# Performance work log

Measured on AMD Instinct MI355X. Metric: run time of the kernel, lower is better.

## Reference

```python
import jax, jax.numpy as jnp
import numpy as np

L, CH, S = 4096, 512, 64
SAMPLE_RATE = 4096.0


def setup_inputs() -> dict:
    key = jax.random.key(0)
    kx, ka, kc = jax.random.split(key, 3)
    x = jax.random.normal(kx, (L, CH), dtype=jnp.float32)
    # original init: lognegA = log(arange(1..S)) broadcast over channels; any real values work
    lognegA = jnp.broadcast_to(jnp.log(jnp.arange(1, S + 1, dtype=jnp.float32)), (CH, S)) \
        + 0.0 * jax.random.normal(ka, (CH, S), dtype=jnp.float32)
    B = jnp.ones((CH, S), dtype=jnp.float32)
    C = 0.01 * jax.random.normal(kc, (CH, S), dtype=jnp.float32)  # nn.initializers.normal() stddev=0.01
    return {"x": x, "lognegA": lognegA, "B": B, "C": C}


def reference(x, lognegA, B, C):
    length = x.shape[0]
    dt = 1.0 / SAMPLE_RATE
    A = -jnp.exp(lognegA)                         # [C, S], strictly negative
    Bd = (jnp.exp(A * dt) - 1.0) * B / A          # discretized B, [C, S]
    # Vandermonde-style kernel: Ak[l, c, s] = exp(l * A[c, s] * dt)
    Ak = jnp.exp(jnp.einsum('l,cs->lcs', jnp.arange(length, dtype=x.dtype), A * dt))
    K = jnp.einsum('cs,lcs->lc', C * Bd, Ak)      # [L, C] per-channel kernel
    # per-channel full causal convolution, truncated to length
    y = jax.vmap(jnp.convolve, in_axes=1, out_axes=1)(x, K)[:length]
    return y
```

## Files before the change

kernel.cpp:

```cpp
#include <hip/hip_runtime.h>


namespace {

constexpr int L_ = 4096;
constexpr int CH_ = 512;
constexpr int S_ = 64;
constexpr float DT = 1.0f / 4096.0f;
constexpr int SC = S_ * CH_;

__global__ void k_params(const float* __restrict__ lognegA,
                         const float* __restrict__ B,
                         const float* __restrict__ C,
                         float* __restrict__ rt, float* __restrict__ wt) {
  const int tid = blockIdx.x * blockDim.x + threadIdx.x;
  const int s = tid >> 9;
  const int c = tid & (CH_ - 1);
  const int i = c * S_ + s;
  const float A = -expf(lognegA[i]);
  const float r = expf(A * DT);
  rt[tid] = r;
  wt[tid] = C[i] * ((r - 1.0f) * B[i] / A);
}

template <int T>
__global__ __launch_bounds__(64) void k_local(const float* __restrict__ x,
                                              const float* __restrict__ rt,
                                              float* __restrict__ carry) {
  const int c = blockIdx.x * 64 + threadIdx.x;
  const int k = blockIdx.y;

  float r[S_], h[S_];
#pragma unroll
  for (int s = 0; s < S_; ++s) {
    r[s] = rt[s * CH_ + c];
    h[s] = 0.0f;
  }

  const float* xp = x + (size_t)k * T * CH_ + c;
#pragma unroll 4
  for (int l = 0; l < T; ++l) {
    const float xv = xp[l * CH_];
#pragma unroll
    for (int s = 0; s < S_; ++s) h[s] = fmaf(r[s], h[s], xv);
  }

  float* cp = carry + (size_t)k * SC + c;
#pragma unroll
  for (int s = 0; s < S_; ++s) cp[s * CH_] = h[s];
}

template <int T, int NC>
__global__ void k_combine(const float* __restrict__ rt,
                          float* __restrict__ carry) {
  const int tid = blockIdx.x * blockDim.x + threadIdx.x;

  const float r = rt[tid];
  float rT = r;
#pragma unroll
  for (int t = 1; t < T; t <<= 1) rT *= rT;

  constexpr int BATCH = (NC < 32) ? NC : 32;
  float state = 0.0f;
  for (int kb = 0; kb < NC; kb += BATCH) {
    float v[BATCH];
#pragma unroll
    for (int j = 0; j < BATCH; ++j) v[j] = carry[(size_t)(kb + j) * SC + tid];
#pragma unroll
    for (int j = 0; j < BATCH; ++j) {
      const float le = v[j];
      v[j] = state;
      state = fmaf(rT, state, le);
    }
#pragma unroll
    for (int j = 0; j < BATCH; ++j) carry[(size_t)(kb + j) * SC + tid] = v[j];
  }
}

template <int T, bool USE_CARRY>
__global__ __launch_bounds__(64) void k_scan_out(const float* __restrict__ x,
                                                 const float* __restrict__ rt,
                                                 const float* __restrict__ wt,
                                                 const float* __restrict__ carry,
                                                 float* __restrict__ y) {
  const int c = blockIdx.x * 64 + threadIdx.x;
  const int k = blockIdx.y;

  float r[S_], w[S_], h[S_];
#pragma unroll
  for (int s = 0; s < S_; ++s) {
    r[s] = rt[s * CH_ + c];
    w[s] = wt[s * CH_ + c];
    h[s] = USE_CARRY ? carry[(size_t)k * SC + s * CH_ + c] : 0.0f;
  }

  const float* xp = x + (size_t)k * T * CH_ + c;
  float* yp = y + (size_t)k * T * CH_ + c;

#pragma unroll 4
  for (int l = 0; l < T; ++l) {
    const float xv = xp[l * CH_];
    float acc[8] = {0, 0, 0, 0, 0, 0, 0, 0};
#pragma unroll
    for (int s = 0; s < S_; ++s) {
      h[s] = fmaf(r[s], h[s], xv);
      acc[s & 7] = fmaf(w[s], h[s], acc[s & 7]);
    }
    yp[l * CH_] = ((acc[0] + acc[4]) + (acc[2] + acc[6])) +
                  ((acc[1] + acc[5]) + (acc[3] + acc[7]));
  }
}

template <int T>
void launch_all(const float* x, const float* la, const float* B, const float* C,
                float* ws, float* y, hipStream_t stream) {
  constexpr int NC = L_ / T;
  float* carry = ws;
  float* rt = ws + (size_t)NC * SC;
  float* wt = rt + SC;

  k_params<<<SC / 256, 256, 0, stream>>>(la, B, C, rt, wt);
  dim3 g(CH_ / 64, NC);
  if (NC > 1) {
    k_local<T><<<g, 64, 0, stream>>>(x, rt, carry);
    k_combine<T, NC><<<SC / 256, 256, 0, stream>>>(rt, carry);
    k_scan_out<T, true><<<g, 64, 0, stream>>>(x, rt, wt, carry, y);
  } else {
    k_scan_out<T, false><<<g, 64, 0, stream>>>(x, rt, wt, carry, y);
  }
}

}

extern "C" void kernel_launch(void* const* d_in, const int* in_sizes, int n_in,
                              void* d_out, int out_size, void* d_ws, size_t ws_size,
                              hipStream_t stream) {
  const float* x = (const float*)d_in[0];
  const float* la = (const float*)d_in[1];
  const float* B = (const float*)d_in[2];
  const float* C = (const float*)d_in[3];
  float* y = (float*)d_out;
  float* ws = (float*)d_ws;

  int NC = 128;
  while (NC > 1 &&
         ((size_t)NC * SC + 2 * SC) * sizeof(float) > ws_size) NC >>= 1;

  switch (L_ / NC) {
    case 32:   launch_all<32>(x, la, B, C, ws, y, stream); break;
    case 64:   launch_all<64>(x, la, B, C, ws, y, stream); break;
    case 128:  launch_all<128>(x, la, B, C, ws, y, stream); break;
    case 256:  launch_all<256>(x, la, B, C, ws, y, stream); break;
    case 512:  launch_all<512>(x, la, B, C, ws, y, stream); break;
    case 1024: launch_all<1024>(x, la, B, C, ws, y, stream); break;
    case 2048: launch_all<2048>(x, la, B, C, ws, y, stream); break;
    default:   launch_all<4096>(x, la, B, C, ws, y, stream); break;
  }
}
```

Before: 95.85 us.

## Split state dimension across four wavefronts and reduce outputs through LDS

The local-scan and output-scan kernels now use 256-thread blocks in which each of four wavefronts owns 16 of the 64 SSM states for the same 64 channels. In the output kernel each wavefront computes partial sums for 8 timesteps, writes them to shared memory, and after a barrier the block adds the four partials and writes y. This cuts per-thread register state from 64 to 16 elements to raise occupancy and parallelism. The cost is redundant x loads per wavefront and two block barriers every 8 timesteps.

Result: faster. 93.82 us (-2.1%).

```diff
diff --git a/kernel.cpp b/kernel.cpp
--- a/kernel.cpp
+++ b/kernel.cpp
@@ -8,6 +8,7 @@
 constexpr int S_ = 64;
 constexpr float DT = 1.0f / 4096.0f;
 constexpr int SC = S_ * CH_;
+constexpr int SG = 16;
 
 __global__ void k_params(const float* __restrict__ lognegA,
                          const float* __restrict__ B,
@@ -24,30 +25,33 @@
 }
 
 template <int T>
-__global__ __launch_bounds__(64) void k_local(const float* __restrict__ x,
-                                              const float* __restrict__ rt,
-                                              float* __restrict__ carry) {
-  const int c = blockIdx.x * 64 + threadIdx.x;
-  const int k = blockIdx.y;
+__global__ __launch_bounds__(256) void k_local_s(const float* __restrict__ x,
+                                                 const float* __restrict__ rt,
+                                                 float* __restrict__ carry) {
+  const int lane = threadIdx.x & 63;
+  const int g = threadIdx.x >> 6;
+  const int k = blockIdx.x >> 3;
+  const int c = ((blockIdx.x & 7) << 6) + lane;
+  const int s0 = g * SG;
 
-  float r[S_], h[S_];
+  float r[SG], h[SG];
 #pragma unroll
-  for (int s = 0; s < S_; ++s) {
-    r[s] = rt[s * CH_ + c];
-    h[s] = 0.0f;
+  for (int i = 0; i < SG; ++i) {
+    r[i] = rt[(s0 + i) * CH_ + c];
+    h[i] = 0.0f;
   }
 
   const float* xp = x + (size_t)k * T * CH_ + c;
-#pragma unroll 4
+#pragma unroll 8
   for (int l = 0; l < T; ++l) {
     const float xv = xp[l * CH_];
 #pragma unroll
-    for (int s = 0; s < S_; ++s) h[s] = fmaf(r[s], h[s], xv);
+    for (int i = 0; i < SG; ++i) h[i] = fmaf(r[i], h[i], xv);
   }
 
-  float* cp = carry + (size_t)k * SC + c;
 #pragma unroll
-  for (int s = 0; s < S_; ++s) cp[s * CH_] = h[s];
+  for (int i = 0; i < SG; ++i)
+    carry[(size_t)k * SC + (s0 + i) * CH_ + c] = h[i];
 }
 
 template <int T, int NC>
@@ -55,8 +59,7 @@
                           float* __restrict__ carry) {
   const int tid = blockIdx.x * blockDim.x + threadIdx.x;
 
-  const float r = rt[tid];
-  float rT = r;
+  float rT = rt[tid];
 #pragma unroll
   for (int t = 1; t < T; t <<= 1) rT *= rT;
 
@@ -78,36 +81,66 @@
 }
 
 template <int T, bool USE_CARRY>
-__global__ __launch_bounds__(64) void k_scan_out(const float* __restrict__ x,
-                                                 const float* __restrict__ rt,
-                                                 const float* __restrict__ wt,
-                                                 const float* __restrict__ carry,
-                                                 float* __restrict__ y) {
-  const int c = blockIdx.x * 64 + threadIdx.x;
-  const int k = blockIdx.y;
+__global__ __launch_bounds__(256) void k_scan_s(const float* __restrict__ x,
+                                                const float* __restrict__ rt,
+                                                const float* __restrict__ wt,
+                                                const float* __restrict__ carry,
+                                                float* __restrict__ y) {
+  __shared__ float lds[4][8][64];
 
-  float r[S_], w[S_], h[S_];
+  const int lane = threadIdx.x & 63;
+  const int g = threadIdx.x >> 6;
+  const int k = blockIdx.x >> 3;
+  const int cb = (blockIdx.x & 7) << 6;
+  const int c = cb + lane;
+  const int s0 = g * SG;
+
+  float r[SG], w[SG], h[SG];
 #pragma unroll
-  for (int s = 0; s < S_; ++s) {
-    r[s] = rt[s * CH_ + c];
-    w[s] = wt[s * CH_ + c];
-    h[s] = USE_CARRY ? carry[(size_t)k * SC + s * CH_ + c] : 0.0f;
+  for (int i = 0; i < SG; ++i) {
+    const int idx = (s0 + i) * CH_ + c;
+    r[i] = rt[idx];
+    w[i] = wt[idx];
+    h[i] = USE_CARRY ? carry[(size_t)k * SC + idx] : 0.0f;
   }
 
   const float* xp = x + (size_t)k * T * CH_ + c;
-  float* yp = y + (size_t)k * T * CH_ + c;
+  float* yp = y + (size_t)k * T * CH_;
 
-#pragma unroll 4
-  for (int l = 0; l < T; ++l) {
-    const float xv = xp[l * CH_];
-    float acc[8] = {0, 0, 0, 0, 0, 0, 0, 0};
+  for (int l = 0; l < T; l += 8) {
+    float part[8];
 #pragma unroll
-    for (int s = 0; s < S_; ++s) {
-      h[s] = fmaf(r[s], h[s], xv);
-      acc[s & 7] = fmaf(w[s], h[s], acc[s & 7]);
+    for (int j = 0; j < 8; ++j) {
+      const float xv = xp[(l + j) * CH_];
+      float a0 = 0, a1 = 0, a2 = 0, a3 = 0;
+#pragma unroll
+      for (int i = 0; i < SG; i += 4) {
+        h[i]     = fmaf(r[i],     h[i],     xv);
+        h[i + 1] = fmaf(r[i + 1], h[i + 1], xv);
+        h[i + 2] = fmaf(r[i + 2], h[i + 2], xv);
+        h[i + 3] = fmaf(r[i + 3], h[i + 3], xv);
+        a0 = fmaf(w[i],     h[i],     a0);
+        a1 = fmaf(w[i + 1], h[i + 1], a1);
+        a2 = fmaf(w[i + 2], h[i + 2], a2);
+        a3 = fmaf(w[i + 3], h[i + 3], a3);
+      }
+      part[j] = (a0 + a1) + (a2 + a3);
     }
-    yp[l * CH_] = ((acc[0] + acc[4]) + (acc[2] + acc[6])) +
-                  ((acc[1] + acc[5]) + (acc[3] + acc[7]));
+
+#pragma unroll
+    for (int j = 0; j < 8; ++j) lds[g][j][lane] = part[j];
+    __syncthreads();
+
+#pragma unroll
+    for (int p = 0; p < 2; ++p) {
+      const int idx = (int)threadIdx.x + p * 256;
+      const int j = idx >> 6;
+      const int ln = idx & 63;
+      const float v = (lds[0][j][ln] + lds[1][j][ln]) +
+                      (lds[2][j][ln] + lds[3][j][ln]);
+      yp[(size_t)(l + j) * CH_ + cb + ln] = v;
+    }
+    __syncthreads();
   }
 }
 
@@ -120,13 +153,12 @@
   float* wt = rt + SC;
 
   k_params<<<SC / 256, 256, 0, stream>>>(la, B, C, rt, wt);
-  dim3 g(CH_ / 64, NC);
   if (NC > 1) {
-    k_local<T><<<g, 64, 0, stream>>>(x, rt, carry);
+    k_local_s<T><<<NC * 8, 256, 0, stream>>>(x, rt, carry);
     k_combine<T, NC><<<SC / 256, 256, 0, stream>>>(rt, carry);
-    k_scan_out<T, true><<<g, 64, 0, stream>>>(x, rt, wt, carry, y);
+    k_scan_s<T, true><<<NC * 8, 256, 0, stream>>>(x, rt, wt, carry, y);
   } else {
-    k_scan_out<T, false><<<g, 64, 0, stream>>>(x, rt, wt, carry, y);
+    k_scan_s<T, false><<<8, 256, 0, stream>>>(x, rt, wt, carry, y);
   }
 }
 
```
